# Optimization experiments

Hardware: AMD Instinct MI355X
Metric: run time of the kernel (lower is better)

The kernel has to match this reference:

```python
import jax, jax.numpy as jnp
import numpy as np

N_NODES = 50000
N_EDGES = 100000
IN_FEATS = 63          # nodes has 64 cols: 63 features + 1 root flag
HIDDEN = 64
NUM_REL = 8
OUT_DIM = 1


def setup_inputs() -> dict:
    key = jax.random.key(0)
    k1, k2, k3, k4, k5, k6, k7 = jax.random.split(key, 7)
    nodes = jax.random.normal(k1, (N_NODES, IN_FEATS + 1), dtype=jnp.float32)
    senders = jax.random.randint(k2, (N_EDGES,), 0, N_NODES, dtype=jnp.int32)
    receivers = jax.random.randint(k3, (N_EDGES,), 0, N_NODES, dtype=jnp.int32)
    edge_types = jax.random.randint(k4, (N_EDGES,), 0, NUM_REL, dtype=jnp.int32)
    n_node = jnp.ones((1,), dtype=jnp.int32) * N_NODES
    # lecun_normal for kernels: std = 1/sqrt(fan_in)
    kernels = jax.random.normal(k5, (NUM_REL, IN_FEATS, HIDDEN), dtype=jnp.float32) / np.sqrt(IN_FEATS)
    dense_w = jax.random.normal(k6, (HIDDEN, OUT_DIM), dtype=jnp.float32) / np.sqrt(HIDDEN)
    dense_b = jnp.zeros((OUT_DIM,), dtype=jnp.float32)
    return {"nodes": nodes, "senders": senders, "receivers": receivers,
            "edge_types": edge_types, "n_node": n_node,
            "kernels": kernels, "dense_w": dense_w, "dense_b": dense_b}


def reference(nodes, senders, receivers, edge_types, n_node, kernels, dense_w, dense_b):
    num_nodes = nodes.shape[0]
    h = nodes[:, :-1]                     # [N, IN_FEATS]
    is_root = nodes[:, -1:]               # [N, 1]

    # --- single RGCN layer (hidden_dims=[64]) ---
    sender_feats = h[senders]             # [E, IN_FEATS] gather
    edge_kernels = kernels[edge_types]    # [E, IN_FEATS, HIDDEN] relation gather
    messages = jnp.einsum('eif,ei->ef', edge_kernels, sender_feats)  # [E, HIDDEN]

    ones = jnp.ones_like(senders, dtype=jnp.float32)
    sender_deg = jax.ops.segment_sum(ones, senders, num_segments=num_nodes)
    receiver_deg = jax.ops.segment_sum(ones, receivers, num_segments=num_nodes)
    norm_s = jax.lax.rsqrt(jnp.maximum(sender_deg, 1.0))
    norm_r = jax.lax.rsqrt(jnp.maximum(receiver_deg, 1.0))

    messages = messages * norm_s[senders, None]
    agg = jax.ops.segment_sum(messages, receivers, num_segments=num_nodes)
    agg = agg * norm_r[:, None]
    h = jax.nn.relu(agg)                  # [N, HIDDEN]

    # --- root pooling (num_graphs == 1) ---
    num_graphs = n_node.shape[0]
    segment_ids = jnp.repeat(jnp.arange(num_graphs), repeats=num_nodes // num_graphs)
    graph_emb = jax.ops.segment_sum(h * is_root, segment_ids, num_segments=num_graphs)  # [1, HIDDEN]

    out = graph_emb @ dense_w + dense_b   # [1, OUT_DIM]
    return jnp.squeeze(out, axis=0)
```

## Files before the change

### kernel.cpp

```cpp
#include <hip/hip_runtime.h>

#define NN 50000
#define NE 100000
#define IN_F 63
#define HID 64
#define NREL 8
#define CHUNK 64

__global__ __launch_bounds__(256) void deg_kernel(const int* __restrict__ senders,
                                                  const int* __restrict__ receivers,
                                                  float* __restrict__ sdeg,
                                                  float* __restrict__ rdeg) {
    int e = blockIdx.x * 256 + threadIdx.x;
    if (e < NE) {
        atomicAdd(&sdeg[senders[e]], 1.0f);
        atomicAdd(&rdeg[receivers[e]], 1.0f);
    }
}

__global__ __launch_bounds__(256, 4) void edge_kernel(const float* __restrict__ nodes,
                                                      const int* __restrict__ senders,
                                                      const int* __restrict__ receivers,
                                                      const int* __restrict__ etypes,
                                                      const float* __restrict__ kernels,
                                                      const float* __restrict__ sdeg,
                                                      float* __restrict__ agg) {
    const int lane = threadIdx.x & 63;
    const int t = blockIdx.x & (NREL - 1);
    const int chunk = (blockIdx.x >> 3) * 4 + (threadIdx.x >> 6);
    const int base = chunk * CHUNK;
    if (base >= NE) return;
    const int lim = min(base + CHUNK, NE);

    float kcol[IN_F];
    const float* Kt = kernels + (size_t)t * IN_F * HID;
#pragma unroll
    for (int i = 0; i < IN_F; ++i) kcol[i] = Kt[i * HID + lane];

    const int e = base + lane;
    int s_l = 0, r_l = 0, ty = -1;
    if (e < lim) {
        ty  = etypes[e];
        s_l = senders[e];
        r_l = receivers[e];
    }
    float ns_l = 1.0f;
    if (ty == t) ns_l = rsqrtf(fmaxf(sdeg[s_l], 1.0f));

    unsigned long long m = __ballot(ty == t);
    while (m) {
        const int i0 = __builtin_ctzll(m); m &= m - 1;
        const bool has2 = (m != 0);
        const int i1 = has2 ? __builtin_ctzll(m) : i0;
        if (has2) m &= m - 1;

        const int   s0  = __builtin_amdgcn_readfirstlane(__shfl(s_l, i0));
        const int   r0  = __builtin_amdgcn_readfirstlane(__shfl(r_l, i0));
        const float ns0 = __shfl(ns_l, i0);
        const int   s1  = __builtin_amdgcn_readfirstlane(__shfl(s_l, i1));
        const int   r1  = __builtin_amdgcn_readfirstlane(__shfl(r_l, i1));
        const float ns1 = __shfl(ns_l, i1);

        const float4* xa = (const float4*)(nodes + (size_t)s0 * (IN_F + 1));
        const float4* xb = (const float4*)(nodes + (size_t)s1 * (IN_F + 1));
        float a0 = 0.f, a1 = 0.f, a2 = 0.f, a3 = 0.f;
        float b0 = 0.f, b1 = 0.f, b2 = 0.f, b3 = 0.f;
#pragma unroll
        for (int j = 0; j < 16; ++j) {
            const float4 va = xa[j];
            const float4 vb = xb[j];
            a0 = fmaf(kcol[4 * j + 0], va.x, a0);
            a1 = fmaf(kcol[4 * j + 1], va.y, a1);
            a2 = fmaf(kcol[4 * j + 2], va.z, a2);
            if (4 * j + 3 < IN_F) a3 = fmaf(kcol[4 * j + 3], va.w, a3);
            b0 = fmaf(kcol[4 * j + 0], vb.x, b0);
            b1 = fmaf(kcol[4 * j + 1], vb.y, b1);
            b2 = fmaf(kcol[4 * j + 2], vb.z, b2);
            if (4 * j + 3 < IN_F) b3 = fmaf(kcol[4 * j + 3], vb.w, b3);
        }
        atomicAdd(&agg[(size_t)r0 * HID + lane], ((a0 + a1) + (a2 + a3)) * ns0);
        if (has2)
            atomicAdd(&agg[(size_t)r1 * HID + lane], ((b0 + b1) + (b2 + b3)) * ns1);
    }
}

__global__ __launch_bounds__(256) void readout_kernel(const float* __restrict__ nodes,
                                                      const float* __restrict__ agg,
                                                      const float* __restrict__ rdeg,
                                                      const float* __restrict__ w,
                                                      const float* __restrict__ b,
                                                      float* __restrict__ out) {
    __shared__ float bsum;
    if (threadIdx.x == 0) bsum = 0.f;
    __syncthreads();

    const int lane = threadIdx.x & 63;
    const int gw = blockIdx.x * 4 + (threadIdx.x >> 6);
    const int nw = gridDim.x * 4;
    const float wf = w[lane];

    float local = 0.f;
    for (int n = gw; n < NN; n += nw) {
        float a = agg[(size_t)n * HID + lane];
        float nr = rsqrtf(fmaxf(rdeg[n], 1.0f));
        float root = nodes[(size_t)n * (IN_F + 1) + IN_F];
        local += fmaxf(a * nr, 0.f) * root;
    }
    float v = local * wf;
#pragma unroll
    for (int o = 32; o > 0; o >>= 1) v += __shfl_xor(v, o, 64);

    if (lane == 0) atomicAdd(&bsum, v);
    __syncthreads();
    if (threadIdx.x == 0) {
        float val = bsum;
        if (blockIdx.x == 0) val += b[0];
        atomicAdd(out, val);
    }
}

extern "C" void kernel_launch(void* const* d_in, const int* in_sizes, int n_in,
                              void* d_out, int out_size, void* d_ws, size_t ws_size,
                              hipStream_t stream) {
    const float* nodes     = (const float*)d_in[0];
    const int*   senders   = (const int*)d_in[1];
    const int*   receivers = (const int*)d_in[2];
    const int*   etypes    = (const int*)d_in[3];
    const float* kernels   = (const float*)d_in[5];
    const float* dense_w   = (const float*)d_in[6];
    const float* dense_b   = (const float*)d_in[7];
    float* out = (float*)d_out;

    float* agg  = (float*)d_ws;
    float* sdeg = agg + (size_t)NN * HID;
    float* rdeg = sdeg + NN;

    size_t zero_bytes = ((size_t)NN * HID + 2 * (size_t)NN) * sizeof(float);
    hipMemsetAsync(d_ws, 0, zero_bytes, stream);
    hipMemsetAsync(d_out, 0, sizeof(float), stream);

    deg_kernel<<<(NE + 255) / 256, 256, 0, stream>>>(senders, receivers, sdeg, rdeg);

    const int nchunks = (NE + CHUNK - 1) / CHUNK;
    const int cgroups = (nchunks + 3) / 4;
    const int blocks  = cgroups * NREL;
    edge_kernel<<<blocks, 256, 0, stream>>>(nodes, senders, receivers, etypes,
                                            kernels, sdeg, agg);

    readout_kernel<<<1024, 256, 0, stream>>>(nodes, agg, rdeg, dense_w, dense_b, out);
}
```

Before: 134.8 us.

## Replace atomic scatter with per-edge message buffer and linked-list receiver gather

The degree kernel now builds per-receiver linked lists via atomicExch instead of counting receiver degree. The message kernel writes each edge's message to a dense per-edge buffer rather than atomically adding into a per-node aggregate. The readout walks each node's list to sum messages and count degree before applying the norm and ReLU. This removes the 12.8MB zeroing memset and the float atomics on aggregates. In exchange it adds a 25.6MB write and read of messages and a serial, dependent pointer-chase per node. The 4th feature weight is zeroed so the root-flag column can be multiplied without a guard.

```diff
diff --git a/kernel.cpp b/kernel.cpp
--- a/kernel.cpp
+++ b/kernel.cpp
@@ -7,24 +7,25 @@
 #define NREL 8
 #define CHUNK 64
 
-__global__ __launch_bounds__(256) void deg_kernel(const int* __restrict__ senders,
-                                                  const int* __restrict__ receivers,
-                                                  float* __restrict__ sdeg,
-                                                  float* __restrict__ rdeg) {
+__global__ __launch_bounds__(256) void deg_link_kernel(const int* __restrict__ senders,
+                                                       const int* __restrict__ receivers,
+                                                       float* __restrict__ sdeg,
+                                                       int* __restrict__ head,
+                                                       int* __restrict__ nxt) {
     int e = blockIdx.x * 256 + threadIdx.x;
     if (e < NE) {
         atomicAdd(&sdeg[senders[e]], 1.0f);
-        atomicAdd(&rdeg[receivers[e]], 1.0f);
+        int old = atomicExch(&head[receivers[e]], e);
+        nxt[e] = old;
     }
 }
 
-__global__ __launch_bounds__(256, 4) void edge_kernel(const float* __restrict__ nodes,
-                                                      const int* __restrict__ senders,
-                                                      const int* __restrict__ receivers,
-                                                      const int* __restrict__ etypes,
-                                                      const float* __restrict__ kernels,
-                                                      const float* __restrict__ sdeg,
-                                                      float* __restrict__ agg) {
+__global__ __launch_bounds__(256, 4) void msg_kernel(const float* __restrict__ nodes,
+                                                     const int* __restrict__ senders,
+                                                     const int* __restrict__ etypes,
+                                                     const float* __restrict__ kernels,
+                                                     const float* __restrict__ sdeg,
+                                                     float* __restrict__ M) {
     const int lane = threadIdx.x & 63;
     const int t = blockIdx.x & (NREL - 1);
     const int chunk = (blockIdx.x >> 3) * 4 + (threadIdx.x >> 6);
@@ -32,17 +33,19 @@
     if (base >= NE) return;
     const int lim = min(base + CHUNK, NE);
 
-    float kcol[IN_F];
+    float kcol[HID];
     const float* Kt = kernels + (size_t)t * IN_F * HID;
 #pragma unroll
     for (int i = 0; i < IN_F; ++i) kcol[i] = Kt[i * HID + lane];
+    kcol[IN_F] = 0.0f;
+#pragma unroll
+    for (int i = 0; i < HID; ++i) asm volatile("" : "+v"(kcol[i]));
 
     const int e = base + lane;
-    int s_l = 0, r_l = 0, ty = -1;
+    int s_l = 0, ty = -1;
     if (e < lim) {
         ty  = etypes[e];
         s_l = senders[e];
-        r_l = receivers[e];
     }
     float ns_l = 1.0f;
     if (ty == t) ns_l = rsqrtf(fmaxf(sdeg[s_l], 1.0f));
@@ -55,14 +58,13 @@
         if (has2) m &= m - 1;
 
         const int   s0  = __builtin_amdgcn_readfirstlane(__shfl(s_l, i0));
-        const int   r0  = __builtin_amdgcn_readfirstlane(__shfl(r_l, i0));
         const float ns0 = __shfl(ns_l, i0);
         const int   s1  = __builtin_amdgcn_readfirstlane(__shfl(s_l, i1));
-        const int   r1  = __builtin_amdgcn_readfirstlane(__shfl(r_l, i1));
         const float ns1 = __shfl(ns_l, i1);
+        const int e0 = base + i0, e1 = base + i1;
 
-        const float4* xa = (const float4*)(nodes + (size_t)s0 * (IN_F + 1));
-        const float4* xb = (const float4*)(nodes + (size_t)s1 * (IN_F + 1));
+        const float4* xa = (const float4*)(nodes + (size_t)s0 * HID);
+        const float4* xb = (const float4*)(nodes + (size_t)s1 * HID);
         float a0 = 0.f, a1 = 0.f, a2 = 0.f, a3 = 0.f;
         float b0 = 0.f, b1 = 0.f, b2 = 0.f, b3 = 0.f;
 #pragma unroll
@@ -72,24 +74,25 @@
             a0 = fmaf(kcol[4 * j + 0], va.x, a0);
             a1 = fmaf(kcol[4 * j + 1], va.y, a1);
             a2 = fmaf(kcol[4 * j + 2], va.z, a2);
-            if (4 * j + 3 < IN_F) a3 = fmaf(kcol[4 * j + 3], va.w, a3);
+            a3 = fmaf(kcol[4 * j + 3], va.w, a3);
             b0 = fmaf(kcol[4 * j + 0], vb.x, b0);
             b1 = fmaf(kcol[4 * j + 1], vb.y, b1);
             b2 = fmaf(kcol[4 * j + 2], vb.z, b2);
-            if (4 * j + 3 < IN_F) b3 = fmaf(kcol[4 * j + 3], vb.w, b3);
+            b3 = fmaf(kcol[4 * j + 3], vb.w, b3);
         }
-        atomicAdd(&agg[(size_t)r0 * HID + lane], ((a0 + a1) + (a2 + a3)) * ns0);
+        M[(size_t)e0 * HID + lane] = ((a0 + a1) + (a2 + a3)) * ns0;
         if (has2)
-            atomicAdd(&agg[(size_t)r1 * HID + lane], ((b0 + b1) + (b2 + b3)) * ns1);
+            M[(size_t)e1 * HID + lane] = ((b0 + b1) + (b2 + b3)) * ns1;
     }
 }
 
-__global__ __launch_bounds__(256) void readout_kernel(const float* __restrict__ nodes,
-                                                      const float* __restrict__ agg,
-                                                      const float* __restrict__ rdeg,
-                                                      const float* __restrict__ w,
-                                                      const float* __restrict__ b,
-                                                      float* __restrict__ out) {
+__global__ __launch_bounds__(256) void gather_kernel(const float* __restrict__ nodes,
+                                                     const float* __restrict__ M,
+                                                     const int* __restrict__ head,
+                                                     const int* __restrict__ nxt,
+                                                     const float* __restrict__ w,
+                                                     const float* __restrict__ b,
+                                                     float* __restrict__ out) {
     __shared__ float bsum;
     if (threadIdx.x == 0) bsum = 0.f;
     __syncthreads();
@@ -99,14 +102,21 @@
     const int nw = gridDim.x * 4;
     const float wf = w[lane];
 
-    float local = 0.f;
+    float part = 0.f;
     for (int n = gw; n < NN; n += nw) {
-        float a = agg[(size_t)n * HID + lane];
-        float nr = rsqrtf(fmaxf(rdeg[n], 1.0f));
-        float root = nodes[(size_t)n * (IN_F + 1) + IN_F];
-        local += fmaxf(a * nr, 0.f) * root;
+        int p = head[n];
+        float acc = 0.f, deg = 0.f;
+        while (p >= 0) {
+            const int pn = nxt[p];
+            acc += M[(size_t)p * HID + lane];
+            deg += 1.f;
+            p = pn;
+        }
+        const float nr = rsqrtf(fmaxf(deg, 1.0f));
+        const float root = nodes[(size_t)n * HID + IN_F];
+        part += fmaxf(acc * nr, 0.f) * root;
     }
-    float v = local * wf;
+    float v = part * wf;
 #pragma unroll
     for (int o = 32; o > 0; o >>= 1) v += __shfl_xor(v, o, 64);
 
@@ -131,21 +141,24 @@
     const float* dense_b   = (const float*)d_in[7];
     float* out = (float*)d_out;
 
-    float* agg  = (float*)d_ws;
-    float* sdeg = agg + (size_t)NN * HID;
-    float* rdeg = sdeg + NN;
+    float* M    = (float*)d_ws;
+    int*   head = (int*)(M + (size_t)NE * HID);
+    int*   nxt  = head + NN;
+    float* sdeg = (float*)(nxt + NE);
 
-    size_t zero_bytes = ((size_t)NN * HID + 2 * (size_t)NN) * sizeof(float);
-    hipMemsetAsync(d_ws, 0, zero_bytes, stream);
+    hipMemsetAsync(head, 0xFF, NN * sizeof(int), stream);
+    hipMemsetAsync(sdeg, 0, NN * sizeof(float), stream);
     hipMemsetAsync(d_out, 0, sizeof(float), stream);
 
-    deg_kernel<<<(NE + 255) / 256, 256, 0, stream>>>(senders, receivers, sdeg, rdeg);
+    deg_link_kernel<<<(NE + 255) / 256, 256, 0, stream>>>(senders, receivers,
+                                                          sdeg, head, nxt);
 
     const int nchunks = (NE + CHUNK - 1) / CHUNK;
     const int cgroups = (nchunks + 3) / 4;
     const int blocks  = cgroups * NREL;
-    edge_kernel<<<blocks, 256, 0, stream>>>(nodes, senders, receivers, etypes,
-                                            kernels, sdeg, agg);
+    msg_kernel<<<blocks, 256, 0, stream>>>(nodes, senders, etypes,
+                                           kernels, sdeg, M);
 
-    readout_kernel<<<1024, 256, 0, stream>>>(nodes, agg, rdeg, dense_w, dense_b, out);
+    gather_kernel<<<2048, 256, 0, stream>>>(nodes, M, head, nxt,
+                                            dense_w, dense_b, out);
 }
```

After: 183.7 us. 36.3% more time.
